# Optimization experiments

Measured on AMD Instinct MI355X. Metric: run time of the kernel, lower is better.

## Reference

```python
import jax, jax.numpy as jnp
import numpy as np

MX, SX = 0.0, 1.0  # msx
MY, SY = 0.0, 1.0  # msy


def _mode_linear(inp, phase, w, b):
    # Equivalent to: w_p = einsum('ji,imk->jmk', phase, w); out = squeeze(inp[:,None,:] @ w_p) + phase @ b
    # Fused blended form avoids the (batch, in, out) per-sample weight intermediate.
    out = jnp.einsum('bd,idh,bi->bh', inp, w, phase)
    return out + phase @ b


def setup_inputs() -> dict:
    key = jax.random.key(0)
    ks = jax.random.split(key, 4)
    B, D_IN, H, D_OUT = 32768, 256, 1024, 64
    x = jax.random.normal(ks[0], (B, D_IN + 2), dtype=jnp.float32)
    w1 = jax.random.normal(ks[1], (2, D_IN, H), dtype=jnp.float32) * 0.05
    b1 = jnp.zeros((2, H), dtype=jnp.float32)
    w2 = jax.random.normal(ks[2], (2, H, H), dtype=jnp.float32) * 0.05
    b2 = jnp.zeros((2, H), dtype=jnp.float32)
    w3 = jax.random.normal(ks[3], (2, H, D_OUT), dtype=jnp.float32) * 0.05
    b3 = jnp.zeros((2, D_OUT), dtype=jnp.float32)
    return {"x": x, "w1": w1, "b1": b1, "w2": w2, "b2": b2, "w3": w3, "b3": b3}


def reference(x, w1, b1, w2, b2, w3, b3):
    phase = x[:, -2:]                 # unscaled phase weights, per original code
    xs = (x - MX) / SX
    h = xs[:, :-2]                    # [B, D_IN]
    out = jax.nn.elu(_mode_linear(h, phase, w1, b1))
    out = jax.nn.elu(_mode_linear(out, phase, w2, b2))
    out = _mode_linear(out, phase, w3, b3)
    return out * SY + MY
```

## Files before the change

### kernel.cpp

```cpp
#include <hip/hip_runtime.h>

typedef unsigned short u16;
typedef __bf16 bf16x8 __attribute__((ext_vector_type(8)));
typedef float f32x4 __attribute__((ext_vector_type(4)));

#define AS1 __attribute__((address_space(1)))
#define AS3 __attribute__((address_space(3)))

static __device__ __forceinline__ u16 f2bf(float f) {
  union { float f; unsigned u; } v; v.f = f;
  unsigned r = (v.u + 0x7fff + ((v.u >> 16) & 1)) >> 16;
  return (u16)r;
}

__global__ void prep_x_kernel(const float* __restrict__ x, u16* __restrict__ hx,
                              float2* __restrict__ phase, int B) {
  int i = blockIdx.x * blockDim.x + threadIdx.x;
  int total = B * 128;
  if (i < total) {
    int row = i >> 7, k2 = (i & 127);
    const float2 v = *reinterpret_cast<const float2*>(x + (size_t)row * 258 + k2 * 2);
    u16 a = f2bf(v.x), b = f2bf(v.y);
    *reinterpret_cast<unsigned*>(hx + (size_t)row * 256 + k2 * 2) =
        (unsigned)a | ((unsigned)b << 16);
  }
  if (i < B) {
    phase[i] = *reinterpret_cast<const float2*>(x + (size_t)i * 258 + 256);
  }
}

__global__ void prep_w_kernel(const float* __restrict__ w, u16* __restrict__ wt,
                              int K, int N) {
  __shared__ u16 tile[64][65];
  int k0 = blockIdx.x * 64, n0 = blockIdx.y * 64, mode = blockIdx.z;
  const float* src = w + (size_t)mode * K * N;
  u16* dst = wt + (size_t)mode * N * K;
  int c = threadIdx.x & 63;
  int r4 = threadIdx.x >> 6;
#pragma unroll
  for (int i = 0; i < 16; ++i) {
    int r = r4 + i * 4;
    tile[r][c] = f2bf(src[(size_t)(k0 + r) * N + n0 + c]);
  }
  __syncthreads();
#pragma unroll
  for (int i = 0; i < 16; ++i) {
    int r = r4 + i * 4;
    dst[(size_t)(n0 + r) * K + k0 + c] = tile[c][r];
  }
}

__global__ void prep_w_int_kernel(const float* __restrict__ w, u16* __restrict__ wt,
                                  int K, int N) {
  __shared__ u16 tile[64][65];
  int k0 = blockIdx.x * 64, n0 = blockIdx.y * 64, mode = blockIdx.z;
  const float* src = w + (size_t)mode * K * N;
  int c = threadIdx.x & 63;
  int r4 = threadIdx.x >> 6;
#pragma unroll
  for (int i = 0; i < 16; ++i) {
    int r = r4 + i * 4;
    tile[r][c] = f2bf(src[(size_t)(k0 + r) * N + n0 + c]);
  }
  __syncthreads();
#pragma unroll
  for (int i = 0; i < 16; ++i) {
    int n = n0 + r4 + i * 4;
    int np = ((n >> 4) << 5) + (mode << 4) + (n & 15);
    wt[(size_t)np * K + k0 + c] = tile[c][r4 + i * 4];
  }
}

template <bool ELU_STORE>
__global__ __launch_bounds__(512, 2) void gemm_ring(
    const u16* __restrict__ A, const u16* __restrict__ Wt,
    const float* __restrict__ bias, const float2* __restrict__ phase,
    u16* __restrict__ out, int K, int Np) {
  __shared__ u16 lds[4][2][8192];
  const int tnc = Np >> 8;
  const int nwg = gridDim.x;
  int id = blockIdx.x;
  const int cpx = nwg >> 3;
  id = (id & 7) * cpx + (id >> 3);
  const int m0 = (id / tnc) * 256;
  const int n0 = (id % tnc) * 256;
  const int t = threadIdx.x;
  const int lane = t & 63;
  const int wave = t >> 6;
  const int wr = wave >> 2, wc = wave & 3;
  const int lr = lane & 15, ks = lane >> 4;
  const int cswz = lr * 64 + (((ks * 8) ^ ((lr >> 3) << 4)) << 1);

  int soff[2];
#pragma unroll
  for (int ld = 0; ld < 2; ++ld) {
    int e = (ld * 512 + t) * 8;
    int st = e >> 9;
    int rl = (e >> 5) & 15;
    int c = e & 31;
    int c0 = c ^ (((rl >> 3) & 1) << 4);
    soff[ld] = (st * 16 + rl) * K + c0;
  }
  const u16* Abase = A + (size_t)m0 * K;
  const u16* Bbase = Wt + (size_t)n0 * K;

  f32x4 acc[8][4] = {};
  const int NT = K >> 5;

  auto stage = [&](int bb, int tile) {
    const int kt = tile << 5;
#pragma unroll
    for (int ld = 0; ld < 2; ++ld)
      __builtin_amdgcn_global_load_lds(
          (const AS1 void*)(Abase + kt + soff[ld]),
          (AS3 void*)(&lds[bb][0][(ld * 512 + t) * 8]), 16, 0, 0);
#pragma unroll
    for (int ld = 0; ld < 2; ++ld)
      __builtin_amdgcn_global_load_lds(
          (const AS1 void*)(Bbase + kt + soff[ld]),
          (AS3 void*)(&lds[bb][1][(ld * 512 + t) * 8]), 16, 0, 0);
  };

#define BAR()                    \
  asm volatile("" ::: "memory"); \
  __builtin_amdgcn_s_barrier();  \
  asm volatile("" ::: "memory");

#define LOADA(mh)                                 \
  _Pragma("unroll") for (int m = 0; m < 4; ++m)   \
      af[m] = *(const bf16x8*)(lA + (((wr * 8 + (mh)*4 + m) << 10) + cswz));
#define LOADB()                                   \
  _Pragma("unroll") for (int n = 0; n < 4; ++n)   \
      bfr[n] = *(const bf16x8*)(lB + (((wc * 4 + n) << 10) + cswz));
#define MFMAH(mh)                                                       \
  __builtin_amdgcn_s_setprio(1);                                        \
  _Pragma("unroll") for (int m = 0; m < 4; ++m)                         \
  _Pragma("unroll") for (int n = 0; n < 4; ++n)                         \
      acc[(mh)*4 + m][n] = __builtin_amdgcn_mfma_f32_16x16x32_bf16(     \
          af[m], bfr[n], acc[(mh)*4 + m][n], 0, 0, 0);                  \
  __builtin_amdgcn_s_setprio(0);

  stage(0, 0);
  stage(1, 1);
  stage(2, 2);
  asm volatile("s_waitcnt vmcnt(8)" ::: "memory");
  BAR();

  for (int tt = 0; tt < NT; ++tt) {
    const char* lA = (const char*)&lds[tt & 3][0][0];
    const char* lB = (const char*)&lds[tt & 3][1][0];
    bf16x8 af[4], bfr[4];
    LOADA(0);
    LOADB();
    if (tt + 3 < NT) stage((tt + 3) & 3, tt + 3);
    BAR();
    __builtin_amdgcn_sched_barrier(0);
    MFMAH(0);
    BAR();
    LOADA(1);
    BAR();
    __builtin_amdgcn_sched_barrier(0);
    MFMAH(1);
    asm volatile("s_waitcnt vmcnt(8)" ::: "memory");
    BAR();
  }
#undef LOADA
#undef LOADB
#undef MFMAH

  const int Nreal = Np >> 1;
  const int colbase = (n0 + wc * 64) >> 1;
  float bias0[2], bias1[2];
#pragma unroll
  for (int pj = 0; pj < 2; ++pj) {
    int ncol = colbase + pj * 16 + lr;
    bias0[pj] = bias[ncol];
    bias1[pj] = bias[Nreal + ncol];
  }
#pragma unroll
  for (int m = 0; m < 8; ++m) {
#pragma unroll
    for (int j = 0; j < 4; ++j) {
      int grow = m0 + wr * 128 + m * 16 + ks * 4 + j;
      float2 ph = phase[grow];
#pragma unroll
      for (int pj = 0; pj < 2; ++pj) {
        int ncol = colbase + pj * 16 + lr;
        float v = ph.x * (acc[m][pj * 2 + 0][j] + bias0[pj]) +
                  ph.y * (acc[m][pj * 2 + 1][j] + bias1[pj]);
        if (ELU_STORE) v = v > 0.f ? v : (__expf(v) - 1.f);
        out[(size_t)grow * Nreal + ncol] = f2bf(v);
      }
    }
  }
#undef BAR
}

template <int BM, int BN, int WM, int WN, bool ELU_BF16>
__launch_bounds__(256, 2) __global__
void gemm_dualmode(const u16* __restrict__ A, const u16* __restrict__ WT,
                   const float* __restrict__ bias, const float2* __restrict__ phase,
                   void* __restrict__ out, int K, int N) {
  constexpr int MF = WM / 16, NF = WN / 16;
  __shared__ u16 ldsA[BM * 32];
  __shared__ u16 ldsB[2][BN * 32];
  const int m0 = blockIdx.x * BM;
  const int n0 = blockIdx.y * BN;
  const int t = threadIdx.x;
  const int wave = t >> 6, lane = t & 63;
  constexpr int NWC = BN / WN;
  const int wr = wave / NWC, wc = wave % NWC;
  const int lr = lane & 15, ks = lane >> 4;

  f32x4 acc[2][MF][NF] = {};

  for (int kt = 0; kt < K; kt += 32) {
#pragma unroll
    for (int i = 0; i < BM / 64; ++i) {
      int tt = t + i * 256;
      int r = tt >> 2, c8 = (tt & 3) * 8;
      __builtin_amdgcn_global_load_lds(
          (const AS1 void*)(A + (size_t)(m0 + r) * K + kt + c8),
          (AS3 void*)(ldsA + (size_t)tt * 8), 16, 0, 0);
    }
#pragma unroll
    for (int md = 0; md < 2; ++md) {
#pragma unroll
      for (int i = 0; i < BN / 64; ++i) {
        int tt = t + i * 256;
        int r = tt >> 2, c8 = (tt & 3) * 8;
        __builtin_amdgcn_global_load_lds(
            (const AS1 void*)(WT + (size_t)md * N * K + (size_t)(n0 + r) * K + kt + c8),
            (AS3 void*)(ldsB[md] + (size_t)tt * 8), 16, 0, 0);
      }
    }
    __syncthreads();

    bf16x8 af[MF], b0f[NF], b1f[NF];
#pragma unroll
    for (int m = 0; m < MF; ++m)
      af[m] = *reinterpret_cast<const bf16x8*>(&ldsA[(wr * WM + m * 16 + lr) * 32 + ks * 8]);
#pragma unroll
    for (int n = 0; n < NF; ++n) {
      b0f[n] = *reinterpret_cast<const bf16x8*>(&ldsB[0][(wc * WN + n * 16 + lr) * 32 + ks * 8]);
      b1f[n] = *reinterpret_cast<const bf16x8*>(&ldsB[1][(wc * WN + n * 16 + lr) * 32 + ks * 8]);
    }
#pragma unroll
    for (int m = 0; m < MF; ++m) {
#pragma unroll
      for (int n = 0; n < NF; ++n) {
        acc[0][m][n] = __builtin_amdgcn_mfma_f32_16x16x32_bf16(af[m], b0f[n], acc[0][m][n], 0, 0, 0);
        acc[1][m][n] = __builtin_amdgcn_mfma_f32_16x16x32_bf16(af[m], b1f[n], acc[1][m][n], 0, 0, 0);
      }
    }
    __syncthreads();
  }

#pragma unroll
  for (int m = 0; m < MF; ++m) {
#pragma unroll
    for (int j = 0; j < 4; ++j) {
      int grow = m0 + wr * WM + m * 16 + ks * 4 + j;
      float2 ph = phase[grow];
#pragma unroll
      for (int n = 0; n < NF; ++n) {
        int gcol = n0 + wc * WN + n * 16 + lr;
        float v = ph.x * (acc[0][m][n][j] + bias[gcol]) +
                  ph.y * (acc[1][m][n][j] + bias[N + gcol]);
        if (ELU_BF16) {
          v = v > 0.f ? v : (__expf(v) - 1.f);
          ((u16*)out)[(size_t)grow * N + gcol] = f2bf(v);
        } else {
          ((float*)out)[(size_t)grow * N + gcol] = v;
        }
      }
    }
  }
}

extern "C" void kernel_launch(void* const* d_in, const int* in_sizes, int n_in,
                              void* d_out, int out_size, void* d_ws, size_t ws_size,
                              hipStream_t stream) {
  const float* x  = (const float*)d_in[0];
  const float* w1 = (const float*)d_in[1];
  const float* b1 = (const float*)d_in[2];
  const float* w2 = (const float*)d_in[3];
  const float* b2 = (const float*)d_in[4];
  const float* w3 = (const float*)d_in[5];
  const float* b3 = (const float*)d_in[6];
  float* out = (float*)d_out;
  const int B = 32768, DIN = 256, H = 1024, DOUT = 64;

  char* ws = (char*)d_ws;
  u16* W1Ti = (u16*)ws;    ws += (size_t)2 * H * DIN * 2;
  u16* W2Ti = (u16*)ws;    ws += (size_t)2 * H * H * 2;
  u16* W3T = (u16*)ws;     ws += (size_t)2 * DOUT * H * 2;
  float2* phase = (float2*)ws; ws += (size_t)B * 8;
  u16* hx = (u16*)ws;      ws += (size_t)B * DIN * 2;
  u16* h1 = (u16*)ws;      ws += (size_t)B * H * 2;
  u16* h2 = (u16*)ws;      ws += (size_t)B * H * 2;

  prep_x_kernel<<<(B * 128 + 255) / 256, 256, 0, stream>>>(x, hx, phase, B);
  prep_w_int_kernel<<<dim3(DIN / 64, H / 64, 2), 256, 0, stream>>>(w1, W1Ti, DIN, H);
  prep_w_int_kernel<<<dim3(H / 64, H / 64, 2), 256, 0, stream>>>(w2, W2Ti, H, H);
  prep_w_kernel<<<dim3(H / 64, DOUT / 64, 2), 256, 0, stream>>>(w3, W3T, H, DOUT);

  const int nwg = (B / 256) * (2 * H / 256);
  gemm_ring<true><<<nwg, 512, 0, stream>>>(hx, W1Ti, b1, phase, h1, DIN, 2 * H);
  gemm_ring<true><<<nwg, 512, 0, stream>>>(h1, W2Ti, b2, phase, h2, H, 2 * H);
  gemm_dualmode<128, 64, 64, 32, false>
      <<<dim3(B / 128, DOUT / 64), 256, 0, stream>>>(h2, W3T, b3, phase, out, H, DOUT);
}
```

Before: 239.7 us.

## Switch dual-mode ring GEMM to 32x32x16 MFMA with 32-column mode interleave

Replaces the 16x16x32 bf16 MFMA tiles in the two large hidden-layer GEMMs with 32x32x16 MFMA tiles. The weight interleave changes from 16 to 32 columns per mode so one 32-wide MFMA output pairs with the other mode's block for the phase blend. LDS fragment addressing and the epilogue row/column mapping are rewritten to match, and the sched_barriers around the MFMA blocks are removed. The goal is fewer LDS fragment reads per FLOP and higher MFMA throughput, at the cost of possible bank conflicts with the unchanged swizzle and different register pressure.

```diff
diff --git a/kernel.cpp b/kernel.cpp
--- a/kernel.cpp
+++ b/kernel.cpp
@@ -3,6 +3,7 @@
 typedef unsigned short u16;
 typedef __bf16 bf16x8 __attribute__((ext_vector_type(8)));
 typedef float f32x4 __attribute__((ext_vector_type(4)));
+typedef float f32x16 __attribute__((ext_vector_type(16)));
 
 #define AS1 __attribute__((address_space(1)))
 #define AS3 __attribute__((address_space(3)))
@@ -66,13 +67,13 @@
 #pragma unroll
   for (int i = 0; i < 16; ++i) {
     int n = n0 + r4 + i * 4;
-    int np = ((n >> 4) << 5) + (mode << 4) + (n & 15);
+    int np = ((n >> 5) << 6) + (mode << 5) + (n & 31);
     wt[(size_t)np * K + k0 + c] = tile[c][r4 + i * 4];
   }
 }
 
 template <bool ELU_STORE>
-__global__ __launch_bounds__(512, 2) void gemm_ring(
+__global__ __launch_bounds__(512, 2) void gemm_ring32(
     const u16* __restrict__ A, const u16* __restrict__ Wt,
     const float* __restrict__ bias, const float2* __restrict__ phase,
     u16* __restrict__ out, int K, int Np) {
@@ -88,8 +89,13 @@
   const int lane = t & 63;
   const int wave = t >> 6;
   const int wr = wave >> 2, wc = wave & 3;
-  const int lr = lane & 15, ks = lane >> 4;
-  const int cswz = lr * 64 + (((ks * 8) ^ ((lr >> 3) << 4)) << 1);
+  const int l31 = lane & 31, lhi = lane >> 5;
+
+  const int sub_l = ((l31 >> 4) & 1) * 1024 + (l31 & 15) * 64;
+  int cx[2];
+#pragma unroll
+  for (int kk = 0; kk < 2; ++kk)
+    cx[kk] = (((kk * 16 + lhi * 8) ^ (((l31 >> 3) & 1) << 4)) << 1);
 
   int soff[2];
 #pragma unroll
@@ -104,7 +110,7 @@
   const u16* Abase = A + (size_t)m0 * K;
   const u16* Bbase = Wt + (size_t)n0 * K;
 
-  f32x4 acc[8][4] = {};
+  f32x16 acc[4][2] = {};
   const int NT = K >> 5;
 
   auto stage = [&](int bb, int tile) {
@@ -126,18 +132,23 @@
   __builtin_amdgcn_s_barrier();  \
   asm volatile("" ::: "memory");
 
-#define LOADA(mh)                                 \
-  _Pragma("unroll") for (int m = 0; m < 4; ++m)   \
-      af[m] = *(const bf16x8*)(lA + (((wr * 8 + (mh)*4 + m) << 10) + cswz));
-#define LOADB()                                   \
-  _Pragma("unroll") for (int n = 0; n < 4; ++n)   \
-      bfr[n] = *(const bf16x8*)(lB + (((wc * 4 + n) << 10) + cswz));
-#define MFMAH(mh)                                                       \
-  __builtin_amdgcn_s_setprio(1);                                        \
-  _Pragma("unroll") for (int m = 0; m < 4; ++m)                         \
-  _Pragma("unroll") for (int n = 0; n < 4; ++n)                         \
-      acc[(mh)*4 + m][n] = __builtin_amdgcn_mfma_f32_16x16x32_bf16(     \
-          af[m], bfr[n], acc[(mh)*4 + m][n], 0, 0, 0);                  \
+#define LOADA(mh)                                                            \
+  _Pragma("unroll") for (int m = 0; m < 2; ++m)                              \
+  _Pragma("unroll") for (int kk = 0; kk < 2; ++kk)                           \
+      af[m][kk] = *(const bf16x8*)(lA +                                      \
+          ((wr * 8 + ((mh)*2 + m) * 2) << 10) + sub_l + cx[kk]);
+#define LOADB()                                                              \
+  _Pragma("unroll") for (int n = 0; n < 2; ++n)                              \
+  _Pragma("unroll") for (int kk = 0; kk < 2; ++kk)                           \
+      bfr[n][kk] = *(const bf16x8*)(lB +                                     \
+          ((wc * 4 + n * 2) << 10) + sub_l + cx[kk]);
+#define MFMAH(mh)                                                            \
+  __builtin_amdgcn_s_setprio(1);                                             \
+  _Pragma("unroll") for (int m = 0; m < 2; ++m)                              \
+  _Pragma("unroll") for (int n = 0; n < 2; ++n)                              \
+  _Pragma("unroll") for (int kk = 0; kk < 2; ++kk)                           \
+      acc[(mh)*2 + m][n] = __builtin_amdgcn_mfma_f32_32x32x16_bf16(          \
+          af[m][kk], bfr[n][kk], acc[(mh)*2 + m][n], 0, 0, 0);               \
   __builtin_amdgcn_s_setprio(0);
 
   stage(0, 0);
@@ -149,17 +160,15 @@
   for (int tt = 0; tt < NT; ++tt) {
     const char* lA = (const char*)&lds[tt & 3][0][0];
     const char* lB = (const char*)&lds[tt & 3][1][0];
-    bf16x8 af[4], bfr[4];
+    bf16x8 af[2][2], bfr[2][2];
     LOADA(0);
     LOADB();
     if (tt + 3 < NT) stage((tt + 3) & 3, tt + 3);
     BAR();
-    __builtin_amdgcn_sched_barrier(0);
     MFMAH(0);
     BAR();
     LOADA(1);
     BAR();
-    __builtin_amdgcn_sched_barrier(0);
     MFMAH(1);
     asm volatile("s_waitcnt vmcnt(8)" ::: "memory");
     BAR();
@@ -169,28 +178,18 @@
 #undef MFMAH
 
   const int Nreal = Np >> 1;
-  const int colbase = (n0 + wc * 64) >> 1;
-  float bias0[2], bias1[2];
-#pragma unroll
-  for (int pj = 0; pj < 2; ++pj) {
-    int ncol = colbase + pj * 16 + lr;
-    bias0[pj] = bias[ncol];
-    bias1[pj] = bias[Nreal + ncol];
-  }
-#pragma unroll
-  for (int m = 0; m < 8; ++m) {
-#pragma unroll
-    for (int j = 0; j < 4; ++j) {
-      int grow = m0 + wr * 128 + m * 16 + ks * 4 + j;
+  const int col = (n0 >> 1) + wc * 32 + l31;
+  const float bias0 = bias[col];
+  const float bias1 = bias[Nreal + col];
+#pragma unroll
+  for (int m = 0; m < 4; ++m) {
+#pragma unroll
+    for (int rg = 0; rg < 16; ++rg) {
+      int grow = m0 + wr * 128 + m * 32 + (rg & 3) + 8 * (rg >> 2) + 4 * lhi;
       float2 ph = phase[grow];
-#pragma unroll
-      for (int pj = 0; pj < 2; ++pj) {
-        int ncol = colbase + pj * 16 + lr;
-        float v = ph.x * (acc[m][pj * 2 + 0][j] + bias0[pj]) +
-                  ph.y * (acc[m][pj * 2 + 1][j] + bias1[pj]);
-        if (ELU_STORE) v = v > 0.f ? v : (__expf(v) - 1.f);
-        out[(size_t)grow * Nreal + ncol] = f2bf(v);
-      }
+      float v = ph.x * (acc[m][0][rg] + bias0) + ph.y * (acc[m][1][rg] + bias1);
+      if (ELU_STORE) v = v > 0.f ? v : (__expf(v) - 1.f);
+      out[(size_t)grow * Nreal + col] = f2bf(v);
     }
   }
 #undef BAR
@@ -306,8 +305,8 @@
   prep_w_kernel<<<dim3(H / 64, DOUT / 64, 2), 256, 0, stream>>>(w3, W3T, H, DOUT);
 
   const int nwg = (B / 256) * (2 * H / 256);
-  gemm_ring<true><<<nwg, 512, 0, stream>>>(hx, W1Ti, b1, phase, h1, DIN, 2 * H);
-  gemm_ring<true><<<nwg, 512, 0, stream>>>(h1, W2Ti, b2, phase, h2, H, 2 * H);
+  gemm_ring32<true><<<nwg, 512, 0, stream>>>(hx, W1Ti, b1, phase, h1, DIN, 2 * H);
+  gemm_ring32<true><<<nwg, 512, 0, stream>>>(h1, W2Ti, b2, phase, h2, H, 2 * H);
   gemm_dualmode<128, 64, 64, 32, false>
       <<<dim3(B / 128, DOUT / 64), 256, 0, stream>>>(h2, W3T, b3, phase, out, H, DOUT);
 }
```

Measured after the change: 263.6 us. +10.0%, slower.

## Software-pipeline LDS fragment loads and cut barriers in GEMM main loop

Applied to the files above, without the earlier changes.

Restructures the K-loop so the next tile's A-lower and B fragments are read from LDS into registers right after the end-of-iteration barrier. The A-upper fragment load is issued just before the first MFMA half so it overlaps. Barriers per iteration drop from four to one, and the vmcnt wait moves between the two MFMA halves. The goal is to hide LDS read latency and remove barrier stalls, at the cost of extra live registers for the double A fragments and a tighter dependence on the 4-deep buffer ring for correctness.

```diff
diff --git a/kernel.cpp b/kernel.cpp
--- a/kernel.cpp
+++ b/kernel.cpp
@@ -126,45 +126,49 @@
   __builtin_amdgcn_s_barrier();  \
   asm volatile("" ::: "memory");
 
-#define LOADA(mh)                                 \
+#define LOADA0(buf)                               \
   _Pragma("unroll") for (int m = 0; m < 4; ++m)   \
-      af[m] = *(const bf16x8*)(lA + (((wr * 8 + (mh)*4 + m) << 10) + cswz));
-#define LOADB()                                   \
+      af0[m] = *(const bf16x8*)((const char*)&lds[buf][0][0] + (((wr * 8 + m) << 10) + cswz));
+#define LOADA1(buf)                               \
+  _Pragma("unroll") for (int m = 0; m < 4; ++m)   \
+      af1[m] = *(const bf16x8*)((const char*)&lds[buf][0][0] + (((wr * 8 + 4 + m) << 10) + cswz));
+#define LOADB(buf)                                \
   _Pragma("unroll") for (int n = 0; n < 4; ++n)   \
-      bfr[n] = *(const bf16x8*)(lB + (((wc * 4 + n) << 10) + cswz));
-#define MFMAH(mh)                                                       \
+      bfr[n] = *(const bf16x8*)((const char*)&lds[buf][1][0] + (((wc * 4 + n) << 10) + cswz));
+#define MFMAH(mh, AF)                                                   \
   __builtin_amdgcn_s_setprio(1);                                        \
   _Pragma("unroll") for (int m = 0; m < 4; ++m)                         \
   _Pragma("unroll") for (int n = 0; n < 4; ++n)                         \
       acc[(mh)*4 + m][n] = __builtin_amdgcn_mfma_f32_16x16x32_bf16(     \
-          af[m], bfr[n], acc[(mh)*4 + m][n], 0, 0, 0);                  \
+          AF[m], bfr[n], acc[(mh)*4 + m][n], 0, 0, 0);                  \
   __builtin_amdgcn_s_setprio(0);
+
+  bf16x8 af0[4], af1[4], bfr[4];
 
   stage(0, 0);
   stage(1, 1);
   stage(2, 2);
   asm volatile("s_waitcnt vmcnt(8)" ::: "memory");
   BAR();
+  LOADA0(0);
+  LOADB(0);
 
   for (int tt = 0; tt < NT; ++tt) {
-    const char* lA = (const char*)&lds[tt & 3][0][0];
-    const char* lB = (const char*)&lds[tt & 3][1][0];
-    bf16x8 af[4], bfr[4];
-    LOADA(0);
-    LOADB();
+    const int b = tt & 3;
+    LOADA1(b);
+    MFMAH(0, af0);
     if (tt + 3 < NT) stage((tt + 3) & 3, tt + 3);
+    asm volatile("s_waitcnt vmcnt(8)" ::: "memory");
+    MFMAH(1, af1);
     BAR();
-    __builtin_amdgcn_sched_barrier(0);
-    MFMAH(0);
-    BAR();
-    LOADA(1);
-    BAR();
-    __builtin_amdgcn_sched_barrier(0);
-    MFMAH(1);
-    asm volatile("s_waitcnt vmcnt(8)" ::: "memory");
-    BAR();
-  }
-#undef LOADA
+    if (tt + 1 < NT) {
+      const int b2 = (tt + 1) & 3;
+      LOADA0(b2);
+      LOADB(b2);
+    }
+  }
+#undef LOADA0
+#undef LOADA1
 #undef LOADB
 #undef MFMAH
 
```

New measurement: 229.8 us. -4.1%, faster.
